# Kernel tuning notes

Measured on AMD Instinct MI355X. Metric: run time of the kernel, lower is better.

## Reference

```python
import jax, jax.numpy as jnp
import numpy as np

HEADS = 4
DIM_HEAD = 32
DIM = 128
EPS = 1e-5


def layer_norm(x, g, b):
    m = jnp.mean(x, axis=-1, keepdims=True)
    v = jnp.var(x, axis=-1, keepdims=True)
    return (x - m) * jax.lax.rsqrt(v + EPS) * g + b


def setup_inputs() -> dict:
    key = jax.random.key(0)
    ks = jax.random.split(key, 24)
    B, D, Hb, Wb = 1, DIM, 50, 50
    N, h, w = 6, 24, 44
    Q = Hb * Wb
    NK = N * h * w
    inner = HEADS * DIM_HEAD
    s = 0.02
    inp = {
        'q': jax.random.normal(ks[0], (B, D, Hb, Wb), jnp.float32),
        'k': jax.random.normal(ks[1], (B, N, D, h, w), jnp.float32),
        'v': jax.random.normal(ks[2], (B, N, D, h, w), jnp.float32),
        'W_logits': jax.random.uniform(ks[3], (B, Q, NK), jnp.float32),
        'vis': jax.random.randint(ks[4], (B, Q, NK), 0, 2, jnp.int32),
        'skip': jax.random.normal(ks[5], (B, D, Hb, Wb), jnp.float32),
        'qn_g': jnp.ones((D,)), 'qn_b': jnp.zeros((D,)),
        'kn_g': jnp.ones((D,)), 'kn_b': jnp.zeros((D,)),
        'vn_g': jnp.ones((D,)), 'vn_b': jnp.zeros((D,)),
        'wq': s * jax.random.normal(ks[6], (inner, D)), 'bq': jnp.zeros((inner,)),
        'wk': s * jax.random.normal(ks[7], (inner, D)), 'bk': jnp.zeros((inner,)),
        'wv': s * jax.random.normal(ks[8], (inner, D)), 'bv': jnp.zeros((inner,)),
        'wproj': s * jax.random.normal(ks[9], (D, inner)), 'bproj': jnp.zeros((D,)),
        'pre_g': jnp.ones((D,)), 'pre_b': jnp.zeros((D,)),
        'w1': s * jax.random.normal(ks[10], (2 * D, D)), 'b1': jnp.zeros((2 * D,)),
        'w2': s * jax.random.normal(ks[11], (D, 2 * D)), 'b2': jnp.zeros((D,)),
        'post_g': jnp.ones((D,)), 'post_b': jnp.zeros((D,)),
    }
    return inp


def reference(q, k, v, W_logits, vis, skip,
              qn_g, qn_b, kn_g, kn_b, vn_g, vn_b,
              wq, bq, wk, bk, wv, bv, wproj, bproj,
              pre_g, pre_b, w1, b1, w2, b2, post_g, post_b):
    B, D, Hb, Wb = q.shape
    Q = Hb * Wb
    scale = DIM_HEAD ** (-0.5)
    # flatten: q -> [B, Q, D]; k,v [B,N,D,h,w] -> [B, NK, D]
    qf = q.reshape(B, D, Q).transpose(0, 2, 1)
    kf = jnp.transpose(k, (0, 1, 3, 4, 2)).reshape(B, -1, D)
    vf = jnp.transpose(v, (0, 1, 3, 4, 2)).reshape(B, -1, D)
    qf = layer_norm(qf, qn_g, qn_b) @ wq.T + bq
    kf = layer_norm(kf, kn_g, kn_b) @ wk.T + bk
    vf = layer_norm(vf, vn_g, vn_b) @ wv.T + bv
    # split heads -> [B, H, Q/K, dh]
    qh = qf.reshape(B, Q, HEADS, DIM_HEAD).transpose(0, 2, 1, 3)
    kh = kf.reshape(B, -1, HEADS, DIM_HEAD).transpose(0, 2, 1, 3)
    vh = vf.reshape(B, -1, HEADS, DIM_HEAD).transpose(0, 2, 1, 3)
    logits = jnp.einsum('bhqd,bhkd->bhqk', qh, kh) * scale
    neg_inf = jnp.finfo(logits.dtype).min
    logits = jnp.where(vis[:, None] == 0, neg_inf, logits)
    logits = logits * W_logits[:, None]
    attn = jax.nn.softmax(logits, axis=-1)
    out = jnp.einsum('bhqk,bhkd->bhqd', attn, vh)
    out = out.transpose(0, 2, 1, 3).reshape(B, Q, HEADS * DIM_HEAD)
    out = out @ wproj.T + bproj
    z = out.transpose(0, 2, 1).reshape(B, D, Hb, Wb) + skip
    zf = z.reshape(B, D, Q).transpose(0, 2, 1)
    zf = layer_norm(zf, pre_g, pre_b)
    hmid = jax.nn.gelu(zf @ w1.T + b1, approximate=False)
    zf = zf + (hmid @ w2.T + b2)
    zf = layer_norm(zf, post_g, post_b)
    return zf.transpose(0, 2, 1).reshape(B, D, Hb, Wb)
```

## Files before the change

kernel.cpp:

```cpp
#include <hip/hip_runtime.h>
#include <hip/hip_bf16.h>

typedef __attribute__((ext_vector_type(8))) short bf16x8;
typedef __attribute__((ext_vector_type(4))) float f32x4;

#define NQ 2500
#define NKK 6336
#define NHEADS 4
#define DHEAD 32
#define SCALE 0.17677669529663687f
#define BIGNEG (-1.0e30f)

#define WS_QP 0
#define WS_KP 640000
#define WS_VT 2262016
#define WS_OP 3884032
#define WS_MP 7724032
#define WS_LP 7844032
#define WS_WB 7964032
#define WS_REQ 8226176

#define WQB 0
#define WKB 16384
#define WVB 32768
#define WPROJB 49152
#define W1B 65536
#define W2B 98304

#define KSPLIT 3
#define SPLIT_LEN 2112
#define TILES_PER_SPLIT 33
#define TQ 16
#define TK 64
#define QBLOCKS 157

#define KSTR 136
#define VSTR 72
#define PSTR 72
#define ABSTR 68

__device__ __forceinline__ unsigned short bf16bits(float x) {
  union { __hip_bfloat16 h; unsigned short s; } cv;
  cv.h = __float2bfloat16(x);
  return cv.s;
}

__global__ __launch_bounds__(256) void wconv_kernel(
    const float* __restrict__ wq, const float* __restrict__ wk,
    const float* __restrict__ wv, const float* __restrict__ wproj,
    const float* __restrict__ w1, const float* __restrict__ w2,
    __hip_bfloat16* __restrict__ wb)
{
  int e = (blockIdx.x * 256 + threadIdx.x) * 4;
  const float* src; int off;
  if (e < 16384)      { src = wq;    off = e; }
  else if (e < 32768) { src = wk;    off = e - 16384; }
  else if (e < 49152) { src = wv;    off = e - 32768; }
  else if (e < 65536) { src = wproj; off = e - 49152; }
  else if (e < 98304) { src = w1;    off = e - 65536; }
  else                { src = w2;    off = e - 98304; }
  float4 v = *(const float4*)(src + off);
  ushort4 o4;
  o4.x = bf16bits(v.x); o4.y = bf16bits(v.y); o4.z = bf16bits(v.z); o4.w = bf16bits(v.w);
  *(ushort4*)((unsigned short*)wb + e) = o4;
}

__global__ __launch_bounds__(128) void lnproj_kernel(
    const float* __restrict__ qin, const float* __restrict__ kin, const float* __restrict__ vin,
    const float* __restrict__ qn_g, const float* __restrict__ qn_b,
    const float* __restrict__ kn_g, const float* __restrict__ kn_b,
    const float* __restrict__ vn_g, const float* __restrict__ vn_b,
    const __hip_bfloat16* __restrict__ wball,
    const float* __restrict__ bq, const float* __restrict__ bk, const float* __restrict__ bv,
    __hip_bfloat16* __restrict__ Qp, __hip_bfloat16* __restrict__ Kp,
    __hip_bfloat16* __restrict__ Vt)
{
  __shared__ __hip_bfloat16 lxb[32][136];
  __shared__ float lpart[32][4][2];
  __shared__ float lmr[32][2];
  __shared__ float lgb[128], lbeb[128];

  const int t = threadIdx.x;
  const int bb = blockIdx.x;
  int mode, row0;
  const float *in, *g, *be, *bo;
  const __hip_bfloat16* wb;
  if (bb < 79)       { mode = 0; row0 = bb * 32;         in = qin; g = qn_g; be = qn_b; wb = wball + WQB; bo = bq; }
  else if (bb < 277) { mode = 1; row0 = (bb - 79) * 32;  in = kin; g = kn_g; be = kn_b; wb = wball + WKB; bo = bk; }
  else               { mode = 2; row0 = (bb - 277) * 32; in = vin; g = vn_g; be = vn_b; wb = wball + WVB; bo = bv; }

  if (t < 128) { lgb[t] = g[t]; lbeb[t] = be[t]; }

  const int row = t & 31, seg = t >> 5;
  int grow = row0 + row;
  size_t base, dstr;
  bool rvalid = true;
  if (mode == 0) { rvalid = (grow < NQ); base = (size_t)(rvalid ? grow : NQ - 1); dstr = NQ; }
  else { int n = grow / 1056, rr = grow - n * 1056; base = (size_t)n * 135168 + rr; dstr = 1056; }

  float xr[32];
  float s = 0.f, ss = 0.f;
  #pragma unroll
  for (int i = 0; i < 32; ++i) {
    float x = in[base + (size_t)(seg * 32 + i) * dstr];
    xr[i] = x; s += x; ss += x * x;
  }
  lpart[row][seg][0] = s; lpart[row][seg][1] = ss;
  __syncthreads();
  if (t < 32) {
    float S  = lpart[t][0][0] + lpart[t][1][0] + lpart[t][2][0] + lpart[t][3][0];
    float SS = lpart[t][0][1] + lpart[t][1][1] + lpart[t][2][1] + lpart[t][3][1];
    float mean = S * (1.f / 128.f);
    float var  = SS * (1.f / 128.f) - mean * mean;
    lmr[t][0] = mean;
    lmr[t][1] = rsqrtf(fmaxf(var, 0.f) + 1e-5f);
  }
  __syncthreads();
  {
    float mean = lmr[row][0], rstd = lmr[row][1];
    #pragma unroll
    for (int i = 0; i < 32; ++i) {
      int d = seg * 32 + i;
      lxb[row][d] = __float2bfloat16((xr[i] - mean) * rstd * lgb[d] + lbeb[d]);
    }
  }
  __syncthreads();

  const int lane = t & 63;
  const int n16 = lane & 15, quad = lane >> 4;
  const int o0 = (t >> 6) * 64;

  f32x4 acc[2][4] = {};
  for (int kt = 0; kt < 4; ++kt) {
    bf16x8 af[2];
    #pragma unroll
    for (int mi = 0; mi < 2; ++mi)
      af[mi] = *(const bf16x8*)&lxb[mi * 16 + n16][kt * 32 + quad * 8];
    #pragma unroll
    for (int ni = 0; ni < 4; ++ni) {
      bf16x8 bw = *(const bf16x8*)(wb + (size_t)(o0 + ni * 16 + n16) * 128 + kt * 32 + quad * 8);
      #pragma unroll
      for (int mi = 0; mi < 2; ++mi)
        acc[mi][ni] = __builtin_amdgcn_mfma_f32_16x16x32_bf16(af[mi], bw, acc[mi][ni], 0, 0, 0);
    }
  }

  float bias[4];
  #pragma unroll
  for (int ni = 0; ni < 4; ++ni) bias[ni] = bo[o0 + ni * 16 + n16];

  #pragma unroll
  for (int mi = 0; mi < 2; ++mi) {
    int gr0 = row0 + mi * 16 + quad * 4;
    if (mode == 2) {
      #pragma unroll
      for (int ni = 0; ni < 4; ++ni) {
        int o = o0 + ni * 16 + n16;
        ushort4 v4;
        v4.x = bf16bits(acc[mi][ni][0] + bias[ni]);
        v4.y = bf16bits(acc[mi][ni][1] + bias[ni]);
        v4.z = bf16bits(acc[mi][ni][2] + bias[ni]);
        v4.w = bf16bits(acc[mi][ni][3] + bias[ni]);
        *(ushort4*)((unsigned short*)Vt + (size_t)o * NKK + gr0) = v4;
      }
    } else {
      #pragma unroll
      for (int rg = 0; rg < 4; ++rg) {
        int gr = gr0 + rg;
        if (mode != 0 || gr < NQ) {
          #pragma unroll
          for (int ni = 0; ni < 4; ++ni) {
            int o = o0 + ni * 16 + n16;
            __hip_bfloat16 b16 = __float2bfloat16(acc[mi][ni][rg] + bias[ni]);
            if (mode == 0) Qp[(size_t)gr * 128 + o] = b16;
            else           Kp[(size_t)gr * 128 + o] = b16;
          }
        }
      }
    }
  }
}

__global__ __launch_bounds__(256, 3) void attn_kernel(
    const __hip_bfloat16* __restrict__ Qp,
    const __hip_bfloat16* __restrict__ Kp,
    const __hip_bfloat16* __restrict__ Vt,
    const float* __restrict__ Wl,
    const int* __restrict__ vis,
    float* __restrict__ Opart, float* __restrict__ Mpart, float* __restrict__ Lpart)
{
  __shared__ alignas(16) __hip_bfloat16 lk[TK * KSTR];
  __shared__ alignas(16) __hip_bfloat16 lv[128 * VSTR];
  __shared__ alignas(16) float sa_[TQ * ABSTR];
  __shared__ alignas(16) float sb_[TQ * ABSTR];
  __shared__ alignas(16) __hip_bfloat16 lp[NHEADS * TQ * PSTR];

  const int t = threadIdx.x;
  const int lane = t & 63;
  const int h = t >> 6;
  const int n16 = lane & 15;
  const int quad = lane >> 4;
  const int q0 = blockIdx.x * TQ;
  const int split = blockIdx.y;
  const int kbase = split * SPLIT_LEN;

  int gqa = q0 + n16; if (gqa >= NQ) gqa = NQ - 1;
  bf16x8 aq = *(const bf16x8*)(Qp + (size_t)gqa * 128 + h * DHEAD + quad * 8);

  const int kr = t >> 2, kc = (t & 3) * 32;
  const int vr = t >> 1, vc = (t & 1) * 32;
  const int e4 = t * 4, qq = e4 >> 6, kkc = e4 & 63;
  int gqe = q0 + qq; if (gqe >= NQ) gqe = NQ - 1;
  const size_t wbase = (size_t)gqe * NKK + kkc;

  uint4 pk0, pk1, pk2, pk3, pv0, pv1, pv2, pv3;
  float4 pw; int4 pvs;

  auto issue = [&](int k0) {
    const uint4* ksrc = (const uint4*)(Kp + (size_t)(k0 + kr) * 128 + kc);
    pk0 = ksrc[0]; pk1 = ksrc[1]; pk2 = ksrc[2]; pk3 = ksrc[3];
    const uint4* vsrc = (const uint4*)(Vt + (size_t)vr * NKK + k0 + vc);
    pv0 = vsrc[0]; pv1 = vsrc[1]; pv2 = vsrc[2]; pv3 = vsrc[3];
    pw  = *(const float4*)(Wl + wbase + k0);
    pvs = *(const int4*)(vis + wbase + k0);
  };
  auto commit = [&]() {
    uint4* kd = (uint4*)&lk[kr * KSTR + kc];
    kd[0] = pk0; kd[1] = pk1; kd[2] = pk2; kd[3] = pk3;
    uint4* vd = (uint4*)&lv[vr * VSTR + vc];
    vd[0] = pv0; vd[1] = pv1; vd[2] = pv2; vd[3] = pv3;
    float wf[4] = {pw.x, pw.y, pw.z, pw.w};
    int vv[4] = {pvs.x, pvs.y, pvs.z, pvs.w};
    #pragma unroll
    for (int j = 0; j < 4; ++j) {
      sa_[qq * ABSTR + kkc + j] = vv[j] ? wf[j] * SCALE : 0.f;
      sb_[qq * ABSTR + kkc + j] = vv[j] ? 0.f : BIGNEG * wf[j];
    }
  };

  f32x4 o0 = {0.f, 0.f, 0.f, 0.f};
  f32x4 o1 = {0.f, 0.f, 0.f, 0.f};
  float m_run[4], l_run[4];
  #pragma unroll
  for (int r = 0; r < 4; ++r) { m_run[r] = BIGNEG; l_run[r] = 0.f; }

  issue(kbase);
  commit();
  __syncthreads();

  for (int kt = 0; kt < TILES_PER_SPLIT; ++kt) {
    if (kt + 1 < TILES_PER_SPLIT) issue(kbase + (kt + 1) * TK);

    f32x4 s[4];
    #pragma unroll
    for (int ks = 0; ks < 4; ++ks) {
      bf16x8 bk = *(const bf16x8*)&lk[(ks * 16 + n16) * KSTR + h * DHEAD + quad * 8];
      f32x4 z = {0.f, 0.f, 0.f, 0.f};
      s[ks] = __builtin_amdgcn_mfma_f32_16x16x32_bf16(aq, bk, z, 0, 0, 0);
    }

    float lvv[4][4];
    #pragma unroll
    for (int ks = 0; ks < 4; ++ks) {
      #pragma unroll
      for (int r = 0; r < 4; ++r) {
        int idx = (quad * 4 + r) * ABSTR + ks * 16 + n16;
        lvv[ks][r] = s[ks][r] * sa_[idx] + sb_[idx];
      }
    }
    float alpha[4];
    #pragma unroll
    for (int r = 0; r < 4; ++r) {
      float tm = fmaxf(fmaxf(lvv[0][r], lvv[1][r]), fmaxf(lvv[2][r], lvv[3][r]));
      tm = fmaxf(tm, __shfl_xor(tm, 1));
      tm = fmaxf(tm, __shfl_xor(tm, 2));
      tm = fmaxf(tm, __shfl_xor(tm, 4));
      tm = fmaxf(tm, __shfl_xor(tm, 8));
      float m_new = fmaxf(m_run[r], tm);
      alpha[r] = __expf(m_run[r] - m_new);
      m_run[r] = m_new;
      float ssum = 0.f;
      #pragma unroll
      for (int ks = 0; ks < 4; ++ks) {
        float p = __expf(fmaxf(lvv[ks][r] - m_new, BIGNEG));
        lvv[ks][r] = p;
        ssum += p;
      }
      ssum += __shfl_xor(ssum, 1);
      ssum += __shfl_xor(ssum, 2);
      ssum += __shfl_xor(ssum, 4);
      ssum += __shfl_xor(ssum, 8);
      l_run[r] = l_run[r] * alpha[r] + ssum;
    }
    #pragma unroll
    for (int ks = 0; ks < 4; ++ks) {
      #pragma unroll
      for (int r = 0; r < 4; ++r)
        lp[h * (TQ * PSTR) + (quad * 4 + r) * PSTR + ks * 16 + n16] = __float2bfloat16(lvv[ks][r]);
    }
    #pragma unroll
    for (int r = 0; r < 4; ++r) { o0[r] *= alpha[r]; o1[r] *= alpha[r]; }

    #pragma unroll
    for (int kk = 0; kk < 2; ++kk) {
      bf16x8 ap  = *(const bf16x8*)&lp[h * (TQ * PSTR) + n16 * PSTR + kk * 32 + quad * 8];
      bf16x8 bv0 = *(const bf16x8*)&lv[(h * DHEAD + n16) * VSTR + kk * 32 + quad * 8];
      bf16x8 bv1 = *(const bf16x8*)&lv[(h * DHEAD + 16 + n16) * VSTR + kk * 32 + quad * 8];
      o0 = __builtin_amdgcn_mfma_f32_16x16x32_bf16(ap, bv0, o0, 0, 0, 0);
      o1 = __builtin_amdgcn_mfma_f32_16x16x32_bf16(ap, bv1, o1, 0, 0, 0);
    }

    if (kt + 1 < TILES_PER_SPLIT) {
      __syncthreads();
      commit();
      __syncthreads();
    }
  }

  #pragma unroll
  for (int r = 0; r < 4; ++r) {
    int gq = q0 + quad * 4 + r;
    if (gq < NQ) {
      size_t ob = (size_t)split * (NQ * 128) + (size_t)gq * 128 + h * DHEAD;
      Opart[ob + n16] = o0[r];
      Opart[ob + 16 + n16] = o1[r];
      if (n16 == 0) {
        Mpart[((size_t)split * NHEADS + h) * NQ + gq] = m_run[r];
        Lpart[((size_t)split * NHEADS + h) * NQ + gq] = l_run[r];
      }
    }
  }
}

__global__ __launch_bounds__(256) void mlp_kernel(
    const float* __restrict__ Opart, const float* __restrict__ Mpart,
    const float* __restrict__ Lpart,
    const float* __restrict__ skip,
    const __hip_bfloat16* __restrict__ wball,
    const float* __restrict__ bproj,
    const float* __restrict__ pre_g, const float* __restrict__ pre_b,
    const float* __restrict__ b1, const float* __restrict__ b2,
    const float* __restrict__ post_g, const float* __restrict__ post_b,
    float* __restrict__ out)
{
  __shared__ __hip_bfloat16 sab[16][136];
  __shared__ __hip_bfloat16 znb[16][136];
  __shared__ float znf[16][132];
  __shared__ __hip_bfloat16 hb[16][264];
  __shared__ float part[16][4][2];

  const __hip_bfloat16* wprojb = wball + WPROJB;
  const __hip_bfloat16* w1b    = wball + W1B;
  const __hip_bfloat16* w2b    = wball + W2B;

  const int t = threadIdx.x;
  const int q0 = blockIdx.x * TQ;

  {
    int row = t >> 4, c0 = (t & 15) * 8;
    int gq = q0 + row; int cq = gq < NQ ? gq : NQ - 1;
    int head = c0 >> 5;
    float m0 = Mpart[(0 * NHEADS + head) * NQ + cq];
    float m1 = Mpart[(1 * NHEADS + head) * NQ + cq];
    float m2 = Mpart[(2 * NHEADS + head) * NQ + cq];
    float mm = fmaxf(m0, fmaxf(m1, m2));
    float e0 = __expf(m0 - mm), e1 = __expf(m1 - mm), e2 = __expf(m2 - mm);
    float ll = Lpart[(0 * NHEADS + head) * NQ + cq] * e0
             + Lpart[(1 * NHEADS + head) * NQ + cq] * e1
             + Lpart[(2 * NHEADS + head) * NQ + cq] * e2;
    float rll = 1.f / fmaxf(ll, 1e-30f);
    const float* p0 = Opart + (size_t)cq * 128 + c0;
    const float* p1 = p0 + (size_t)NQ * 128;
    const float* p2 = p1 + (size_t)NQ * 128;
    #pragma unroll
    for (int i = 0; i < 8; i += 4) {
      float4 a = *(const float4*)(p0 + i);
      float4 b = *(const float4*)(p1 + i);
      float4 c = *(const float4*)(p2 + i);
      sab[row][c0 + i + 0] = __float2bfloat16((a.x * e0 + b.x * e1 + c.x * e2) * rll);
      sab[row][c0 + i + 1] = __float2bfloat16((a.y * e0 + b.y * e1 + c.y * e2) * rll);
      sab[row][c0 + i + 2] = __float2bfloat16((a.z * e0 + b.z * e1 + c.z * e2) * rll);
      sab[row][c0 + i + 3] = __float2bfloat16((a.w * e0 + b.w * e1 + c.w * e2) * rll);
    }
  }
  __syncthreads();

  const int wid = t >> 6, lane = t & 63;
  const int n16 = lane & 15, quad = lane >> 4;
  const int qrow0 = q0 + quad * 4;

  f32x4 acc1[2] = {};
  for (int kt = 0; kt < 4; ++kt) {
    bf16x8 af = *(const bf16x8*)&sab[n16][kt * 32 + quad * 8];
    #pragma unroll
    for (int ni = 0; ni < 2; ++ni) {
      int o = wid * 32 + ni * 16 + n16;
      bf16x8 bw = *(const bf16x8*)(wprojb + (size_t)o * 128 + kt * 32 + quad * 8);
      acc1[ni] = __builtin_amdgcn_mfma_f32_16x16x32_bf16(af, bw, acc1[ni], 0, 0, 0);
    }
  }
  float z[2][4];
  #pragma unroll
  for (int ni = 0; ni < 2; ++ni) {
    int o = wid * 32 + ni * 16 + n16;
    float bo = bproj[o];
    if (qrow0 + 3 < NQ) {
      float4 sk = *(const float4*)(skip + (size_t)o * NQ + qrow0);
      z[ni][0] = acc1[ni][0] + bo + sk.x;
      z[ni][1] = acc1[ni][1] + bo + sk.y;
      z[ni][2] = acc1[ni][2] + bo + sk.z;
      z[ni][3] = acc1[ni][3] + bo + sk.w;
    } else {
      #pragma unroll
      for (int rg = 0; rg < 4; ++rg) {
        int cq = qrow0 + rg < NQ ? qrow0 + rg : NQ - 1;
        z[ni][rg] = acc1[ni][rg] + bo + skip[(size_t)o * NQ + cq];
      }
    }
  }
  #pragma unroll
  for (int rg = 0; rg < 4; ++rg) {
    float s = z[0][rg] + z[1][rg];
    float ss = z[0][rg] * z[0][rg] + z[1][rg] * z[1][rg];
    s += __shfl_xor(s, 1);  ss += __shfl_xor(ss, 1);
    s += __shfl_xor(s, 2);  ss += __shfl_xor(ss, 2);
    s += __shfl_xor(s, 4);  ss += __shfl_xor(ss, 4);
    s += __shfl_xor(s, 8);  ss += __shfl_xor(ss, 8);
    if (n16 == 0) { part[quad * 4 + rg][wid][0] = s; part[quad * 4 + rg][wid][1] = ss; }
  }
  __syncthreads();
  #pragma unroll
  for (int rg = 0; rg < 4; ++rg) {
    int row = quad * 4 + rg;
    float S  = part[row][0][0] + part[row][1][0] + part[row][2][0] + part[row][3][0];
    float SS = part[row][0][1] + part[row][1][1] + part[row][2][1] + part[row][3][1];
    float mean = S * (1.f / 128.f);
    float var  = SS * (1.f / 128.f) - mean * mean;
    float rstd = rsqrtf(fmaxf(var, 0.f) + 1e-5f);
    #pragma unroll
    for (int ni = 0; ni < 2; ++ni) {
      int o = wid * 32 + ni * 16 + n16;
      float zn = (z[ni][rg] - mean) * rstd * pre_g[o] + pre_b[o];
      znf[row][o] = zn;
      znb[row][o] = __float2bfloat16(zn);
    }
  }
  __syncthreads();

  f32x4 acc2[4] = {};
  for (int kt = 0; kt < 4; ++kt) {
    bf16x8 af = *(const bf16x8*)&znb[n16][kt * 32 + quad * 8];
    #pragma unroll
    for (int ni = 0; ni < 4; ++ni) {
      int j = wid * 64 + ni * 16 + n16;
      bf16x8 bw = *(const bf16x8*)(w1b + (size_t)j * 128 + kt * 32 + quad * 8);
      acc2[ni] = __builtin_amdgcn_mfma_f32_16x16x32_bf16(af, bw, acc2[ni], 0, 0, 0);
    }
  }
  #pragma unroll
  for (int ni = 0; ni < 4; ++ni) {
    int j = wid * 64 + ni * 16 + n16;
    float bj = b1[j];
    #pragma unroll
    for (int rg = 0; rg < 4; ++rg) {
      float a1 = acc2[ni][rg] + bj;
      hb[quad * 4 + rg][j] = __float2bfloat16(0.5f * a1 * (1.0f + erff(a1 * 0.70710678118654752f)));
    }
  }
  __syncthreads();

  f32x4 acc3[2] = {};
  for (int kt = 0; kt < 8; ++kt) {
    bf16x8 af = *(const bf16x8*)&hb[n16][kt * 32 + quad * 8];
    #pragma unroll
    for (int ni = 0; ni < 2; ++ni) {
      int o = wid * 32 + ni * 16 + n16;
      bf16x8 bw = *(const bf16x8*)(w2b + (size_t)o * 256 + kt * 32 + quad * 8);
      acc3[ni] = __builtin_amdgcn_mfma_f32_16x16x32_bf16(af, bw, acc3[ni], 0, 0, 0);
    }
  }
  float y[2][4];
  #pragma unroll
  for (int ni = 0; ni < 2; ++ni) {
    int o = wid * 32 + ni * 16 + n16;
    float bo = b2[o];
    #pragma unroll
    for (int rg = 0; rg < 4; ++rg)
      y[ni][rg] = znf[quad * 4 + rg][o] + acc3[ni][rg] + bo;
  }
  #pragma unroll
  for (int rg = 0; rg < 4; ++rg) {
    float s = y[0][rg] + y[1][rg];
    float ss = y[0][rg] * y[0][rg] + y[1][rg] * y[1][rg];
    s += __shfl_xor(s, 1);  ss += __shfl_xor(ss, 1);
    s += __shfl_xor(s, 2);  ss += __shfl_xor(ss, 2);
    s += __shfl_xor(s, 4);  ss += __shfl_xor(ss, 4);
    s += __shfl_xor(s, 8);  ss += __shfl_xor(ss, 8);
    if (n16 == 0) { part[quad * 4 + rg][wid][0] = s; part[quad * 4 + rg][wid][1] = ss; }
  }
  __syncthreads();
  #pragma unroll
  for (int rg = 0; rg < 4; ++rg) {
    int row = quad * 4 + rg;
    float S  = part[row][0][0] + part[row][1][0] + part[row][2][0] + part[row][3][0];
    float SS = part[row][0][1] + part[row][1][1] + part[row][2][1] + part[row][3][1];
    float mean = S * (1.f / 128.f);
    float var  = SS * (1.f / 128.f) - mean * mean;
    float rstd = rsqrtf(fmaxf(var, 0.f) + 1e-5f);
    #pragma unroll
    for (int ni = 0; ni < 2; ++ni) {
      int o = wid * 32 + ni * 16 + n16;
      y[ni][rg] = (y[ni][rg] - mean) * rstd * post_g[o] + post_b[o];
    }
  }
  #pragma unroll
  for (int ni = 0; ni < 2; ++ni) {
    int o = wid * 32 + ni * 16 + n16;
    if (qrow0 + 3 < NQ) {
      *(float4*)(out + (size_t)o * NQ + qrow0) = make_float4(y[ni][0], y[ni][1], y[ni][2], y[ni][3]);
    } else {
      #pragma unroll
      for (int rg = 0; rg < 4; ++rg)
        if (qrow0 + rg < NQ) out[(size_t)o * NQ + qrow0 + rg] = y[ni][rg];
    }
  }
}

extern "C" void kernel_launch(void* const* d_in, const int* in_sizes, int n_in,
                              void* d_out, int out_size, void* d_ws, size_t ws_size,
                              hipStream_t stream) {
  if (ws_size < (size_t)WS_REQ) return;

  const float* q     = (const float*)d_in[0];
  const float* k     = (const float*)d_in[1];
  const float* v     = (const float*)d_in[2];
  const float* Wl    = (const float*)d_in[3];
  const int*   vis   = (const int*)d_in[4];
  const float* skip  = (const float*)d_in[5];
  const float* qn_g  = (const float*)d_in[6];
  const float* qn_b  = (const float*)d_in[7];
  const float* kn_g  = (const float*)d_in[8];
  const float* kn_b  = (const float*)d_in[9];
  const float* vn_g  = (const float*)d_in[10];
  const float* vn_b  = (const float*)d_in[11];
  const float* wq    = (const float*)d_in[12];
  const float* bq    = (const float*)d_in[13];
  const float* wk    = (const float*)d_in[14];
  const float* bk    = (const float*)d_in[15];
  const float* wv    = (const float*)d_in[16];
  const float* bv    = (const float*)d_in[17];
  const float* wproj = (const float*)d_in[18];
  const float* bproj = (const float*)d_in[19];
  const float* pre_g = (const float*)d_in[20];
  const float* pre_b = (const float*)d_in[21];
  const float* w1    = (const float*)d_in[22];
  const float* b1    = (const float*)d_in[23];
  const float* w2    = (const float*)d_in[24];
  const float* b2    = (const float*)d_in[25];
  const float* post_g= (const float*)d_in[26];
  const float* post_b= (const float*)d_in[27];

  char* ws = (char*)d_ws;
  __hip_bfloat16* Qp = (__hip_bfloat16*)(ws + WS_QP);
  __hip_bfloat16* Kp = (__hip_bfloat16*)(ws + WS_KP);
  __hip_bfloat16* Vt = (__hip_bfloat16*)(ws + WS_VT);
  float* Opart = (float*)(ws + WS_OP);
  float* Mpart = (float*)(ws + WS_MP);
  float* Lpart = (float*)(ws + WS_LP);
  __hip_bfloat16* Wb = (__hip_bfloat16*)(ws + WS_WB);

  hipLaunchKernelGGL(wconv_kernel, dim3(128), dim3(256), 0, stream,
                     wq, wk, wv, wproj, w1, w2, Wb);

  hipLaunchKernelGGL(lnproj_kernel, dim3(475), dim3(128), 0, stream,
                     q, k, v, qn_g, qn_b, kn_g, kn_b, vn_g, vn_b,
                     Wb, bq, bk, bv, Qp, Kp, Vt);

  hipLaunchKernelGGL(attn_kernel, dim3(QBLOCKS, KSPLIT), dim3(256), 0, stream,
                     Qp, Kp, Vt, Wl, vis, Opart, Mpart, Lpart);

  hipLaunchKernelGGL(mlp_kernel, dim3(QBLOCKS), dim3(256), 0, stream,
                     Opart, Mpart, Lpart, skip, Wb, bproj, pre_g, pre_b,
                     b1, b2, post_g, post_b, (float*)d_out);
}
```

Before: 261.6 us.

## Raise attention key split to six, double-buffer prefetch, widen LN-projection blocks

The attention kernel now splits the key range across up to six blocks when the workspace allows, which raises the grid from 471 to 942 blocks to fill the GPU better. It also prefetches two tiles ahead using alternating register sets and a barrier that waits only on LDS counters. The partial outputs and their max and sum values are packed into one row layout, and the merge kernel generalises to a variable split count. The LN-projection kernel uses 256 threads per block with less work per thread. In exchange it uses more registers, which may lower occupancy, writes more partial-result traffic, and drops the clamp inside the exp.

```diff
diff --git a/kernel.cpp b/kernel.cpp
--- a/kernel.cpp
+++ b/kernel.cpp
@@ -14,11 +14,12 @@
 #define WS_QP 0
 #define WS_KP 640000
 #define WS_VT 2262016
-#define WS_OP 3884032
-#define WS_MP 7724032
-#define WS_LP 7844032
-#define WS_WB 7964032
-#define WS_REQ 8226176
+#define WS_WB 3884032
+#define WS_OP 4146176
+#define OSPLIT_F 340000
+#define OROW_F 136
+#define WS_REQ3 8226176ULL
+#define WS_REQ6 12306176ULL
 
 #define WQB 0
 #define WKB 16384
@@ -27,9 +28,7 @@
 #define W1B 65536
 #define W2B 98304
 
-#define KSPLIT 3
-#define SPLIT_LEN 2112
-#define TILES_PER_SPLIT 33
+#define NTILES_TOTAL 99
 #define TQ 16
 #define TK 64
 #define QBLOCKS 157
@@ -43,6 +42,13 @@
   union { __hip_bfloat16 h; unsigned short s; } cv;
   cv.h = __float2bfloat16(x);
   return cv.s;
+}
+
+__device__ __forceinline__ void barrier_lds_only() {
+  asm volatile("" ::: "memory");
+  __builtin_amdgcn_s_waitcnt(0xC07F);
+  __builtin_amdgcn_s_barrier();
+  asm volatile("" ::: "memory");
 }
 
 __global__ __launch_bounds__(256) void wconv_kernel(
@@ -65,7 +71,7 @@
   *(ushort4*)((unsigned short*)wb + e) = o4;
 }
 
-__global__ __launch_bounds__(128) void lnproj_kernel(
+__global__ __launch_bounds__(256) void lnproj_kernel(
     const float* __restrict__ qin, const float* __restrict__ kin, const float* __restrict__ vin,
     const float* __restrict__ qn_g, const float* __restrict__ qn_b,
     const float* __restrict__ kn_g, const float* __restrict__ kn_b,
@@ -76,7 +82,7 @@
     __hip_bfloat16* __restrict__ Vt)
 {
   __shared__ __hip_bfloat16 lxb[32][136];
-  __shared__ float lpart[32][4][2];
+  __shared__ float lpart[32][8][2];
   __shared__ float lmr[32][2];
   __shared__ float lgb[128], lbeb[128];
 
@@ -98,18 +104,19 @@
   if (mode == 0) { rvalid = (grow < NQ); base = (size_t)(rvalid ? grow : NQ - 1); dstr = NQ; }
   else { int n = grow / 1056, rr = grow - n * 1056; base = (size_t)n * 135168 + rr; dstr = 1056; }
 
-  float xr[32];
+  float xr[16];
   float s = 0.f, ss = 0.f;
   #pragma unroll
-  for (int i = 0; i < 32; ++i) {
-    float x = in[base + (size_t)(seg * 32 + i) * dstr];
+  for (int i = 0; i < 16; ++i) {
+    float x = in[base + (size_t)(seg * 16 + i) * dstr];
     xr[i] = x; s += x; ss += x * x;
   }
   lpart[row][seg][0] = s; lpart[row][seg][1] = ss;
   __syncthreads();
   if (t < 32) {
-    float S  = lpart[t][0][0] + lpart[t][1][0] + lpart[t][2][0] + lpart[t][3][0];
-    float SS = lpart[t][0][1] + lpart[t][1][1] + lpart[t][2][1] + lpart[t][3][1];
+    float S = 0.f, SS = 0.f;
+    #pragma unroll
+    for (int j = 0; j < 8; ++j) { S += lpart[t][j][0]; SS += lpart[t][j][1]; }
     float mean = S * (1.f / 128.f);
     float var  = SS * (1.f / 128.f) - mean * mean;
     lmr[t][0] = mean;
@@ -119,43 +126,43 @@
   {
     float mean = lmr[row][0], rstd = lmr[row][1];
     #pragma unroll
-    for (int i = 0; i < 32; ++i) {
-      int d = seg * 32 + i;
+    for (int i = 0; i < 16; ++i) {
+      int d = seg * 16 + i;
       lxb[row][d] = __float2bfloat16((xr[i] - mean) * rstd * lgb[d] + lbeb[d]);
     }
   }
   __syncthreads();
 
-  const int lane = t & 63;
+  const int wid = t >> 6, lane = t & 63;
   const int n16 = lane & 15, quad = lane >> 4;
-  const int o0 = (t >> 6) * 64;
-
-  f32x4 acc[2][4] = {};
+  const int ow = wid * 32;
+
+  f32x4 acc[2][2] = {};
   for (int kt = 0; kt < 4; ++kt) {
     bf16x8 af[2];
     #pragma unroll
     for (int mi = 0; mi < 2; ++mi)
       af[mi] = *(const bf16x8*)&lxb[mi * 16 + n16][kt * 32 + quad * 8];
     #pragma unroll
-    for (int ni = 0; ni < 4; ++ni) {
-      bf16x8 bw = *(const bf16x8*)(wb + (size_t)(o0 + ni * 16 + n16) * 128 + kt * 32 + quad * 8);
+    for (int ni = 0; ni < 2; ++ni) {
+      bf16x8 bw = *(const bf16x8*)(wb + (size_t)(ow + ni * 16 + n16) * 128 + kt * 32 + quad * 8);
       #pragma unroll
       for (int mi = 0; mi < 2; ++mi)
         acc[mi][ni] = __builtin_amdgcn_mfma_f32_16x16x32_bf16(af[mi], bw, acc[mi][ni], 0, 0, 0);
     }
   }
 
-  float bias[4];
-  #pragma unroll
-  for (int ni = 0; ni < 4; ++ni) bias[ni] = bo[o0 + ni * 16 + n16];
+  float bias[2];
+  #pragma unroll
+  for (int ni = 0; ni < 2; ++ni) bias[ni] = bo[ow + ni * 16 + n16];
 
   #pragma unroll
   for (int mi = 0; mi < 2; ++mi) {
     int gr0 = row0 + mi * 16 + quad * 4;
     if (mode == 2) {
       #pragma unroll
-      for (int ni = 0; ni < 4; ++ni) {
-        int o = o0 + ni * 16 + n16;
+      for (int ni = 0; ni < 2; ++ni) {
+        int o = ow + ni * 16 + n16;
         ushort4 v4;
         v4.x = bf16bits(acc[mi][ni][0] + bias[ni]);
         v4.y = bf16bits(acc[mi][ni][1] + bias[ni]);
@@ -169,8 +176,8 @@
         int gr = gr0 + rg;
         if (mode != 0 || gr < NQ) {
           #pragma unroll
-          for (int ni = 0; ni < 4; ++ni) {
-            int o = o0 + ni * 16 + n16;
+          for (int ni = 0; ni < 2; ++ni) {
+            int o = ow + ni * 16 + n16;
             __hip_bfloat16 b16 = __float2bfloat16(acc[mi][ni][rg] + bias[ni]);
             if (mode == 0) Qp[(size_t)gr * 128 + o] = b16;
             else           Kp[(size_t)gr * 128 + o] = b16;
@@ -187,7 +194,7 @@
     const __hip_bfloat16* __restrict__ Vt,
     const float* __restrict__ Wl,
     const int* __restrict__ vis,
-    float* __restrict__ Opart, float* __restrict__ Mpart, float* __restrict__ Lpart)
+    float* __restrict__ Opart)
 {
   __shared__ alignas(16) __hip_bfloat16 lk[TK * KSTR];
   __shared__ alignas(16) __hip_bfloat16 lv[128 * VSTR];
@@ -202,7 +209,9 @@
   const int quad = lane >> 4;
   const int q0 = blockIdx.x * TQ;
   const int split = blockIdx.y;
-  const int kbase = split * SPLIT_LEN;
+  const int ksplit = gridDim.y;
+  const int tstart = (NTILES_TOTAL * split) / ksplit;
+  const int ntiles = (NTILES_TOTAL * (split + 1)) / ksplit - tstart;
 
   int gqa = q0 + n16; if (gqa >= NQ) gqa = NQ - 1;
   bf16x8 aq = *(const bf16x8*)(Qp + (size_t)gqa * 128 + h * DHEAD + quad * 8);
@@ -213,29 +222,52 @@
   int gqe = q0 + qq; if (gqe >= NQ) gqe = NQ - 1;
   const size_t wbase = (size_t)gqe * NKK + kkc;
 
-  uint4 pk0, pk1, pk2, pk3, pv0, pv1, pv2, pv3;
-  float4 pw; int4 pvs;
-
-  auto issue = [&](int k0) {
+  uint4 Ak0, Ak1, Ak2, Ak3, Av0, Av1, Av2, Av3; float4 Aw; int4 Avs;
+  uint4 Bk0, Bk1, Bk2, Bk3, Bv0, Bv1, Bv2, Bv3; float4 Bw; int4 Bvs;
+
+  auto issueA = [&](int tile) {
+    int k0 = (tstart + tile) * TK;
     const uint4* ksrc = (const uint4*)(Kp + (size_t)(k0 + kr) * 128 + kc);
-    pk0 = ksrc[0]; pk1 = ksrc[1]; pk2 = ksrc[2]; pk3 = ksrc[3];
+    Ak0 = ksrc[0]; Ak1 = ksrc[1]; Ak2 = ksrc[2]; Ak3 = ksrc[3];
     const uint4* vsrc = (const uint4*)(Vt + (size_t)vr * NKK + k0 + vc);
-    pv0 = vsrc[0]; pv1 = vsrc[1]; pv2 = vsrc[2]; pv3 = vsrc[3];
-    pw  = *(const float4*)(Wl + wbase + k0);
-    pvs = *(const int4*)(vis + wbase + k0);
+    Av0 = vsrc[0]; Av1 = vsrc[1]; Av2 = vsrc[2]; Av3 = vsrc[3];
+    Aw  = *(const float4*)(Wl + wbase + k0);
+    Avs = *(const int4*)(vis + wbase + k0);
   };
-  auto commit = [&]() {
+  auto issueB = [&](int tile) {
+    int k0 = (tstart + tile) * TK;
+    const uint4* ksrc = (const uint4*)(Kp + (size_t)(k0 + kr) * 128 + kc);
+    Bk0 = ksrc[0]; Bk1 = ksrc[1]; Bk2 = ksrc[2]; Bk3 = ksrc[3];
+    const uint4* vsrc = (const uint4*)(Vt + (size_t)vr * NKK + k0 + vc);
+    Bv0 = vsrc[0]; Bv1 = vsrc[1]; Bv2 = vsrc[2]; Bv3 = vsrc[3];
+    Bw  = *(const float4*)(Wl + wbase + k0);
+    Bvs = *(const int4*)(vis + wbase + k0);
+  };
+  auto commitA = [&]() {
     uint4* kd = (uint4*)&lk[kr * KSTR + kc];
-    kd[0] = pk0; kd[1] = pk1; kd[2] = pk2; kd[3] = pk3;
+    kd[0] = Ak0; kd[1] = Ak1; kd[2] = Ak2; kd[3] = Ak3;
     uint4* vd = (uint4*)&lv[vr * VSTR + vc];
-    vd[0] = pv0; vd[1] = pv1; vd[2] = pv2; vd[3] = pv3;
-    float wf[4] = {pw.x, pw.y, pw.z, pw.w};
-    int vv[4] = {pvs.x, pvs.y, pvs.z, pvs.w};
-    #pragma unroll
-    for (int j = 0; j < 4; ++j) {
-      sa_[qq * ABSTR + kkc + j] = vv[j] ? wf[j] * SCALE : 0.f;
-      sb_[qq * ABSTR + kkc + j] = vv[j] ? 0.f : BIGNEG * wf[j];
-    }
+    vd[0] = Av0; vd[1] = Av1; vd[2] = Av2; vd[3] = Av3;
+    float4 a4, b4;
+    a4.x = Avs.x ? Aw.x * SCALE : 0.f;  b4.x = Avs.x ? 0.f : BIGNEG * Aw.x;
+    a4.y = Avs.y ? Aw.y * SCALE : 0.f;  b4.y = Avs.y ? 0.f : BIGNEG * Aw.y;
+    a4.z = Avs.z ? Aw.z * SCALE : 0.f;  b4.z = Avs.z ? 0.f : BIGNEG * Aw.z;
+    a4.w = Avs.w ? Aw.w * SCALE : 0.f;  b4.w = Avs.w ? 0.f : BIGNEG * Aw.w;
+    *(float4*)&sa_[qq * ABSTR + kkc] = a4;
+    *(float4*)&sb_[qq * ABSTR + kkc] = b4;
+  };
+  auto commitB = [&]() {
+    uint4* kd = (uint4*)&lk[kr * KSTR + kc];
+    kd[0] = Bk0; kd[1] = Bk1; kd[2] = Bk2; kd[3] = Bk3;
+    uint4* vd = (uint4*)&lv[vr * VSTR + vc];
+    vd[0] = Bv0; vd[1] = Bv1; vd[2] = Bv2; vd[3] = Bv3;
+    float4 a4, b4;
+    a4.x = Bvs.x ? Bw.x * SCALE : 0.f;  b4.x = Bvs.x ? 0.f : BIGNEG * Bw.x;
+    a4.y = Bvs.y ? Bw.y * SCALE : 0.f;  b4.y = Bvs.y ? 0.f : BIGNEG * Bw.y;
+    a4.z = Bvs.z ? Bw.z * SCALE : 0.f;  b4.z = Bvs.z ? 0.f : BIGNEG * Bw.z;
+    a4.w = Bvs.w ? Bw.w * SCALE : 0.f;  b4.w = Bvs.w ? 0.f : BIGNEG * Bw.w;
+    *(float4*)&sa_[qq * ABSTR + kkc] = a4;
+    *(float4*)&sb_[qq * ABSTR + kkc] = b4;
   };
 
   f32x4 o0 = {0.f, 0.f, 0.f, 0.f};
@@ -244,13 +276,7 @@
   #pragma unroll
   for (int r = 0; r < 4; ++r) { m_run[r] = BIGNEG; l_run[r] = 0.f; }
 
-  issue(kbase);
-  commit();
-  __syncthreads();
-
-  for (int kt = 0; kt < TILES_PER_SPLIT; ++kt) {
-    if (kt + 1 < TILES_PER_SPLIT) issue(kbase + (kt + 1) * TK);
-
+  auto compute = [&]() {
     f32x4 s[4];
     #pragma unroll
     for (int ks = 0; ks < 4; ++ks) {
@@ -258,7 +284,6 @@
       f32x4 z = {0.f, 0.f, 0.f, 0.f};
       s[ks] = __builtin_amdgcn_mfma_f32_16x16x32_bf16(aq, bk, z, 0, 0, 0);
     }
-
     float lvv[4][4];
     #pragma unroll
     for (int ks = 0; ks < 4; ++ks) {
@@ -282,7 +307,7 @@
       float ssum = 0.f;
       #pragma unroll
       for (int ks = 0; ks < 4; ++ks) {
-        float p = __expf(fmaxf(lvv[ks][r] - m_new, BIGNEG));
+        float p = __expf(lvv[ks][r] - m_new);
         lvv[ks][r] = p;
         ssum += p;
       }
@@ -300,7 +325,6 @@
     }
     #pragma unroll
     for (int r = 0; r < 4; ++r) { o0[r] *= alpha[r]; o1[r] *= alpha[r]; }
-
     #pragma unroll
     for (int kk = 0; kk < 2; ++kk) {
       bf16x8 ap  = *(const bf16x8*)&lp[h * (TQ * PSTR) + n16 * PSTR + kk * 32 + quad * 8];
@@ -309,32 +333,46 @@
       o0 = __builtin_amdgcn_mfma_f32_16x16x32_bf16(ap, bv0, o0, 0, 0, 0);
       o1 = __builtin_amdgcn_mfma_f32_16x16x32_bf16(ap, bv1, o1, 0, 0, 0);
     }
-
-    if (kt + 1 < TILES_PER_SPLIT) {
-      __syncthreads();
-      commit();
-      __syncthreads();
-    }
+  };
+
+  issueA(0);
+  if (ntiles > 1) issueB(1);
+  commitA();
+  barrier_lds_only();
+
+  int kt = 0;
+  while (true) {
+    if (kt + 2 < ntiles) issueA(kt + 2);
+    compute();
+    if (++kt >= ntiles) break;
+    barrier_lds_only();
+    commitB();
+    barrier_lds_only();
+    if (kt + 2 < ntiles) issueB(kt + 2);
+    compute();
+    if (++kt >= ntiles) break;
+    barrier_lds_only();
+    commitA();
+    barrier_lds_only();
   }
 
   #pragma unroll
   for (int r = 0; r < 4; ++r) {
     int gq = q0 + quad * 4 + r;
     if (gq < NQ) {
-      size_t ob = (size_t)split * (NQ * 128) + (size_t)gq * 128 + h * DHEAD;
-      Opart[ob + n16] = o0[r];
-      Opart[ob + 16 + n16] = o1[r];
+      float* rowp = Opart + (size_t)split * OSPLIT_F + (size_t)gq * OROW_F;
+      rowp[h * DHEAD + n16] = o0[r];
+      rowp[h * DHEAD + 16 + n16] = o1[r];
       if (n16 == 0) {
-        Mpart[((size_t)split * NHEADS + h) * NQ + gq] = m_run[r];
-        Lpart[((size_t)split * NHEADS + h) * NQ + gq] = l_run[r];
+        rowp[128 + 2 * h] = m_run[r];
+        rowp[129 + 2 * h] = l_run[r];
       }
     }
   }
 }
 
 __global__ __launch_bounds__(256) void mlp_kernel(
-    const float* __restrict__ Opart, const float* __restrict__ Mpart,
-    const float* __restrict__ Lpart,
+    const float* __restrict__ Opart, int ksplit,
     const float* __restrict__ skip,
     const __hip_bfloat16* __restrict__ wball,
     const float* __restrict__ bproj,
@@ -360,28 +398,35 @@
     int row = t >> 4, c0 = (t & 15) * 8;
     int gq = q0 + row; int cq = gq < NQ ? gq : NQ - 1;
     int head = c0 >> 5;
-    float m0 = Mpart[(0 * NHEADS + head) * NQ + cq];
-    float m1 = Mpart[(1 * NHEADS + head) * NQ + cq];
-    float m2 = Mpart[(2 * NHEADS + head) * NQ + cq];
-    float mm = fmaxf(m0, fmaxf(m1, m2));
-    float e0 = __expf(m0 - mm), e1 = __expf(m1 - mm), e2 = __expf(m2 - mm);
-    float ll = Lpart[(0 * NHEADS + head) * NQ + cq] * e0
-             + Lpart[(1 * NHEADS + head) * NQ + cq] * e1
-             + Lpart[(2 * NHEADS + head) * NQ + cq] * e2;
+    float ms[6], ls[6];
+    #pragma unroll
+    for (int s = 0; s < 6; ++s) {
+      if (s < ksplit) {
+        const float* rp = Opart + (size_t)s * OSPLIT_F + (size_t)cq * OROW_F;
+        ms[s] = rp[128 + 2 * head]; ls[s] = rp[129 + 2 * head];
+      } else { ms[s] = BIGNEG; ls[s] = 0.f; }
+    }
+    float mm = BIGNEG;
+    #pragma unroll
+    for (int s = 0; s < 6; ++s) mm = fmaxf(mm, ms[s]);
+    float es[6]; float ll = 0.f;
+    #pragma unroll
+    for (int s = 0; s < 6; ++s) { es[s] = (s < ksplit) ? __expf(ms[s] - mm) : 0.f; ll += ls[s] * es[s]; }
     float rll = 1.f / fmaxf(ll, 1e-30f);
-    const float* p0 = Opart + (size_t)cq * 128 + c0;
-    const float* p1 = p0 + (size_t)NQ * 128;
-    const float* p2 = p1 + (size_t)NQ * 128;
-    #pragma unroll
-    for (int i = 0; i < 8; i += 4) {
-      float4 a = *(const float4*)(p0 + i);
-      float4 b = *(const float4*)(p1 + i);
-      float4 c = *(const float4*)(p2 + i);
-      sab[row][c0 + i + 0] = __float2bfloat16((a.x * e0 + b.x * e1 + c.x * e2) * rll);
-      sab[row][c0 + i + 1] = __float2bfloat16((a.y * e0 + b.y * e1 + c.y * e2) * rll);
-      sab[row][c0 + i + 2] = __float2bfloat16((a.z * e0 + b.z * e1 + c.z * e2) * rll);
-      sab[row][c0 + i + 3] = __float2bfloat16((a.w * e0 + b.w * e1 + c.w * e2) * rll);
-    }
+    float acc8[8] = {};
+    #pragma unroll
+    for (int s = 0; s < 6; ++s) {
+      if (s < ksplit) {
+        const float* rp = Opart + (size_t)s * OSPLIT_F + (size_t)cq * OROW_F + c0;
+        float4 a = *(const float4*)(rp);
+        float4 b = *(const float4*)(rp + 4);
+        acc8[0] += a.x * es[s]; acc8[1] += a.y * es[s]; acc8[2] += a.z * es[s]; acc8[3] += a.w * es[s];
+        acc8[4] += b.x * es[s]; acc8[5] += b.y * es[s]; acc8[6] += b.z * es[s]; acc8[7] += b.w * es[s];
+      }
+    }
+    #pragma unroll
+    for (int i = 0; i < 8; ++i)
+      sab[row][c0 + i] = __float2bfloat16(acc8[i] * rll);
   }
   __syncthreads();
 
@@ -529,7 +574,8 @@
 extern "C" void kernel_launch(void* const* d_in, const int* in_sizes, int n_in,
                               void* d_out, int out_size, void* d_ws, size_t ws_size,
                               hipStream_t stream) {
-  if (ws_size < (size_t)WS_REQ) return;
+  if (ws_size < WS_REQ3) return;
+  const int ksplit = (ws_size >= WS_REQ6) ? 6 : 3;
 
   const float* q     = (const float*)d_in[0];
   const float* k     = (const float*)d_in[1];
@@ -564,22 +610,20 @@
   __hip_bfloat16* Qp = (__hip_bfloat16*)(ws + WS_QP);
   __hip_bfloat16* Kp = (__hip_bfloat16*)(ws + WS_KP);
   __hip_bfloat16* Vt = (__hip_bfloat16*)(ws + WS_VT);
+  __hip_bfloat16* Wb = (__hip_bfloat16*)(ws + WS_WB);
   float* Opart = (float*)(ws + WS_OP);
-  float* Mpart = (float*)(ws + WS_MP);
-  float* Lpart = (float*)(ws + WS_LP);
-  __hip_bfloat16* Wb = (__hip_bfloat16*)(ws + WS_WB);
 
   hipLaunchKernelGGL(wconv_kernel, dim3(128), dim3(256), 0, stream,
                      wq, wk, wv, wproj, w1, w2, Wb);
 
-  hipLaunchKernelGGL(lnproj_kernel, dim3(475), dim3(128), 0, stream,
+  hipLaunchKernelGGL(lnproj_kernel, dim3(475), dim3(256), 0, stream,
                      q, k, v, qn_g, qn_b, kn_g, kn_b, vn_g, vn_b,
                      Wb, bq, bk, bv, Qp, Kp, Vt);
 
-  hipLaunchKernelGGL(attn_kernel, dim3(QBLOCKS, KSPLIT), dim3(256), 0, stream,
-                     Qp, Kp, Vt, Wl, vis, Opart, Mpart, Lpart);
+  hipLaunchKernelGGL(attn_kernel, dim3(QBLOCKS, ksplit), dim3(256), 0, stream,
+                     Qp, Kp, Vt, Wl, vis, Opart);
 
   hipLaunchKernelGGL(mlp_kernel, dim3(QBLOCKS), dim3(256), 0, stream,
-                     Opart, Mpart, Lpart, skip, Wb, bproj, pre_g, pre_b,
+                     Opart, ksplit, skip, Wb, bproj, pre_g, pre_b,
                      b1, b2, post_g, post_b, (float*)d_out);
 }
```

After: 278.8 us. 1.07x slower.
